# Optimization experiments

Hardware: AMD Instinct MI355X
Metric: run time of the kernel (lower is better)

The kernel has to match this reference:

```python
import jax, jax.numpy as jnp
import numpy as np

N, K = 10000, 32          # nodes, max neighbors
NUM_ELEM = 100
D_ATOM = 128              # atom embedding size
D_DIR_IN, D_DIR = 10, 64  # node direction expansion -> embedding
D_DIST_IN, D_DIST = 128, 128  # edge distance expansion -> embedding


def setup_inputs() -> dict:
    key = jax.random.key(0)
    ks = jax.random.split(key, 12)
    inp = {
        "atomic_numbers": jax.random.randint(ks[0], (N,), 0, NUM_ELEM),
        "node_direction_expansion": jax.random.normal(ks[1], (N, D_DIR_IN), jnp.float32),
        "edge_distance_expansion": jax.random.normal(ks[2], (N, K, D_DIST_IN), jnp.float32),
        "neighbor_list": jax.random.randint(ks[3], (N, K), 0, N),
        "neighbor_mask": jax.random.randint(ks[4], (N, K), 0, 2).astype(bool),
        # learned params
        "src_atom_emb": jax.random.uniform(ks[5], (NUM_ELEM, D_ATOM), jnp.float32, -0.001, 0.001),
        "tgt_atom_emb": jax.random.uniform(ks[6], (NUM_ELEM, D_ATOM), jnp.float32, -0.001, 0.001),
        "src_dir_W": jax.random.normal(ks[7], (D_DIR_IN, D_DIR), jnp.float32) * 0.1,
        "src_dir_b": jnp.zeros((D_DIR,), jnp.float32),
        "tgt_dir_W": jax.random.normal(ks[8], (D_DIR_IN, D_DIR), jnp.float32) * 0.1,
        "tgt_dir_b": jnp.zeros((D_DIR,), jnp.float32),
        "dist_W": jax.random.normal(ks[9], (D_DIST_IN, D_DIST), jnp.float32) * 0.1,
        "dist_b": jnp.zeros((D_DIST,), jnp.float32),
    }
    return inp


def reference(atomic_numbers, node_direction_expansion, edge_distance_expansion,
              neighbor_list, neighbor_mask,
              src_atom_emb, tgt_atom_emb,
              src_dir_W, src_dir_b, tgt_dir_W, tgt_dir_b, dist_W, dist_b):
    # per-node embeddings
    sa = src_atom_emb[atomic_numbers]                      # [N, D_ATOM]
    ta = tgt_atom_emb[atomic_numbers]                      # [N, D_ATOM]
    sd = jax.nn.silu(node_direction_expansion @ src_dir_W + src_dir_b)  # [N, D_DIR]
    td = jax.nn.silu(node_direction_expansion @ tgt_dir_W + tgt_dir_b)  # [N, D_DIR]

    # map_sender_receiver_feature: sender gathered via neighbor_list, receiver broadcast
    sender_atom = sa[neighbor_list]                        # [N, K, D_ATOM]
    recv_atom = jnp.broadcast_to(ta[:, None, :], (N, K, D_ATOM))
    sender_dir = sd[neighbor_list]                         # [N, K, D_DIR]
    recv_dir = jnp.broadcast_to(td[:, None, :], (N, K, D_DIR))

    edist = jax.nn.silu(edge_distance_expansion @ dist_W + dist_b)  # [N, K, D_DIST]

    edge_features = jnp.concatenate(
        [edist, sender_dir, sender_atom, recv_dir, recv_atom], axis=-1)  # [N, K, 512]

    # masked mean over neighbors
    m = neighbor_mask.astype(edge_features.dtype)          # [N, K]
    count = m.sum(axis=1, keepdims=True) + 1e-5            # [N, 1]
    out = (edge_features * m[:, :, None]).sum(axis=1) / count  # [N, 512]
    return out
```

## Files before the change

### kernel.cpp

```cpp
#include <hip/hip_runtime.h>
#include <hip/hip_bf16.h>

#define NN 10000
#define KK 32
#define DDIRIN 10
#define DDIR 64
#define DD 128
#define NODE_BLOCKS 2500

typedef short bf16x8 __attribute__((ext_vector_type(8)));
typedef float f32x4  __attribute__((ext_vector_type(4)));

__device__ __forceinline__ float silu_f(float x) { return x / (1.0f + __expf(-x)); }

__device__ __forceinline__ short f2bf(float f) {
    union { float f; unsigned u; } v; v.f = f;
    unsigned r = (v.u + 0x7fffu + ((v.u >> 16) & 1u)) >> 16;
    return (short)r;
}

__global__ __launch_bounds__(256) void dir_kernel(
    const float* __restrict__ nde,
    const float* __restrict__ sW, const float* __restrict__ sb,
    const float* __restrict__ tW, const float* __restrict__ tb,
    float* __restrict__ sd, float* __restrict__ td)
{
    int gid = blockIdx.x * 256 + threadIdx.x;
    if (gid >= NN * DDIR) return;
    int n = gid >> 6, d = gid & 63;
    float a = sb[d], t = tb[d];
    const float* x = nde + n * DDIRIN;
#pragma unroll
    for (int i = 0; i < DDIRIN; ++i) {
        float xv = x[i];
        a = fmaf(xv, sW[i * DDIR + d], a);
        t = fmaf(xv, tW[i * DDIR + d], t);
    }
    sd[gid] = silu_f(a);
    td[gid] = silu_f(t);
}

template<bool USE_WS>
__global__ __launch_bounds__(256) void gnn_mfma_kernel(
    const int*   __restrict__ an,
    const float* __restrict__ nde,
    const float* __restrict__ edist,
    const int*   __restrict__ nl,
    const int*   __restrict__ nmask,
    const float* __restrict__ semb,
    const float* __restrict__ temb,
    const float* __restrict__ sW, const float* __restrict__ sb,
    const float* __restrict__ tW, const float* __restrict__ tb,
    const float* __restrict__ dW, const float* __restrict__ db,
    const float* __restrict__ sd_ws,
    const float* __restrict__ td_ws,
    float* __restrict__ out)
{
    const int tid  = threadIdx.x;
    const int wid  = tid >> 6;
    const int lane = tid & 63;
    const int l15  = lane & 15;
    const int quad = lane >> 4;

    __shared__ __align__(16) short s_E[32 * 128];
    __shared__ int   s_nl[KK];
    __shared__ float s_mask[KK];
    __shared__ int   s_annl[KK];
    __shared__ float s_sd[USE_WS ? 1 : KK * (DDIR + 4)];
    __shared__ float s_nde[USE_WS ? 1 : KK * DDIRIN];
    __shared__ float s_td[DDIR];

    bf16x8 bfrag[2][4];
    float  bias[2];
#pragma unroll
    for (int c2 = 0; c2 < 2; ++c2) {
        int ncol = (2 * wid + c2) * 16 + l15;
        bias[c2] = db[ncol];
#pragma unroll
        for (int t = 0; t < 4; ++t) {
            bf16x8 v;
#pragma unroll
            for (int j = 0; j < 8; ++j)
                v[j] = f2bf(dW[(t * 32 + quad * 8 + j) * DD + ncol]);
            bfrag[c2][t] = v;
        }
    }

    for (int n = blockIdx.x; n < NN; n += NODE_BLOCKS) {
        __syncthreads();

        if (tid < KK) {
            int j = nl[n * KK + tid];
            s_nl[tid]   = j;
            s_mask[tid] = (nmask[n * KK + tid] != 0) ? 1.0f : 0.0f;
            s_annl[tid] = an[j];
        }
        {
            const float4* E4 = reinterpret_cast<const float4*>(edist + (size_t)n * (KK * DD));
            int row = tid >> 3;
            int cb0 = (tid & 7) * 2;
            float4 a = E4[tid * 4 + 0], b = E4[tid * 4 + 1];
            float4 c = E4[tid * 4 + 2], d = E4[tid * 4 + 3];
            bf16x8 v0, v1;
            v0[0] = f2bf(a.x); v0[1] = f2bf(a.y); v0[2] = f2bf(a.z); v0[3] = f2bf(a.w);
            v0[4] = f2bf(b.x); v0[5] = f2bf(b.y); v0[6] = f2bf(b.z); v0[7] = f2bf(b.w);
            v1[0] = f2bf(c.x); v1[1] = f2bf(c.y); v1[2] = f2bf(c.z); v1[3] = f2bf(c.w);
            v1[4] = f2bf(d.x); v1[5] = f2bf(d.y); v1[6] = f2bf(d.z); v1[7] = f2bf(d.w);
            int sw0 = (cb0     ) ^ (row & 7);
            int sw1 = (cb0 + 1 ) ^ (row & 7);
            *reinterpret_cast<bf16x8*>(&s_E[row * 128 + sw0 * 8]) = v0;
            *reinterpret_cast<bf16x8*>(&s_E[row * 128 + sw1 * 8]) = v1;
        }
        __syncthreads();

        float cnt = 0.0f;
#pragma unroll
        for (int k = 0; k < KK; ++k) cnt += s_mask[k];
        const float inv = 1.0f / (cnt + 1e-5f);
        const float self_scale = cnt * inv;
        float* outn = out + (size_t)n * 512;

        bf16x8 afrag[2][4];
#pragma unroll
        for (int rt = 0; rt < 2; ++rt)
#pragma unroll
            for (int t = 0; t < 4; ++t) {
                int r  = rt * 16 + l15;
                int cb = (t * 4 + quad) ^ (l15 & 7);
                afrag[rt][t] = *reinterpret_cast<const bf16x8*>(&s_E[r * 128 + cb * 8]);
            }
        f32x4 acc[2][2] = {{{0.f,0.f,0.f,0.f},{0.f,0.f,0.f,0.f}},
                           {{0.f,0.f,0.f,0.f},{0.f,0.f,0.f,0.f}}};
#pragma unroll
        for (int t = 0; t < 4; ++t)
#pragma unroll
            for (int rt = 0; rt < 2; ++rt) {
                acc[rt][0] = __builtin_amdgcn_mfma_f32_16x16x32_bf16(afrag[rt][t], bfrag[0][t], acc[rt][0], 0, 0, 0);
                acc[rt][1] = __builtin_amdgcn_mfma_f32_16x16x32_bf16(afrag[rt][t], bfrag[1][t], acc[rt][1], 0, 0, 0);
            }

#pragma unroll
        for (int c2 = 0; c2 < 2; ++c2) {
            float p = 0.0f;
#pragma unroll
            for (int rt = 0; rt < 2; ++rt)
#pragma unroll
                for (int rg = 0; rg < 4; ++rg)
                    p += s_mask[rt * 16 + quad * 4 + rg] * silu_f(acc[rt][c2][rg] + bias[c2]);
            p += __shfl_xor(p, 16);
            p += __shfl_xor(p, 32);
            if (quad == c2) outn[(2 * wid + c2) * 16 + l15] = p * inv;
        }

        if constexpr (!USE_WS) {
            for (int idx = tid; idx < KK * DDIRIN; idx += 256) {
                int k = idx / DDIRIN, i = idx - k * DDIRIN;
                s_nde[k * DDIRIN + i] = nde[s_nl[k] * DDIRIN + i];
            }
            __syncthreads();
            {
                int k = tid >> 3, d0 = (tid & 7) * 8;
                float a8[8];
#pragma unroll
                for (int d = 0; d < 8; ++d) a8[d] = sb[d0 + d];
#pragma unroll
                for (int i = 0; i < DDIRIN; ++i) {
                    float x = s_nde[k * DDIRIN + i];
#pragma unroll
                    for (int d = 0; d < 8; ++d)
                        a8[d] = fmaf(x, sW[i * DDIR + d0 + d], a8[d]);
                }
#pragma unroll
                for (int d = 0; d < 8; ++d) s_sd[k * (DDIR + 4) + d0 + d] = silu_f(a8[d]);
            }
            if (tid < DDIR) {
                float a = tb[tid];
#pragma unroll
                for (int i = 0; i < DDIRIN; ++i)
                    a = fmaf(nde[n * DDIRIN + i], tW[i * DDIR + tid], a);
                s_td[tid] = silu_f(a);
            }
            __syncthreads();
        }

        if (tid < 64) {
            float s = 0.0f;
            if constexpr (USE_WS) {
#pragma unroll 4
                for (int k = 0; k < KK; ++k)
                    s += s_mask[k] * sd_ws[s_nl[k] * DDIR + tid];
            } else {
#pragma unroll
                for (int k = 0; k < KK; ++k)
                    s += s_mask[k] * s_sd[k * (DDIR + 4) + tid];
            }
            outn[128 + tid] = s * inv;
        } else if (tid < 192) {
            int d = tid - 64;
            float s = 0.0f;
#pragma unroll 4
            for (int k = 0; k < KK; ++k)
                s += s_mask[k] * semb[s_annl[k] * DD + d];
            outn[192 + d] = s * inv;
        } else {
            int d = tid - 192;
            float tdv;
            if constexpr (USE_WS) tdv = td_ws[n * DDIR + d];
            else                  tdv = s_td[d];
            outn[320 + d] = tdv * self_scale;
        }
        if (tid < 128)
            outn[384 + tid] = temb[an[n] * DD + tid] * self_scale;
    }
}

extern "C" void kernel_launch(void* const* d_in, const int* in_sizes, int n_in,
                              void* d_out, int out_size, void* d_ws, size_t ws_size,
                              hipStream_t stream) {
    const int*   an    = (const int*)  d_in[0];
    const float* nde   = (const float*)d_in[1];
    const float* edist = (const float*)d_in[2];
    const int*   nl    = (const int*)  d_in[3];
    const int*   nmask = (const int*)  d_in[4];
    const float* semb  = (const float*)d_in[5];
    const float* temb  = (const float*)d_in[6];
    const float* sW    = (const float*)d_in[7];
    const float* sb    = (const float*)d_in[8];
    const float* tW    = (const float*)d_in[9];
    const float* tb    = (const float*)d_in[10];
    const float* dW    = (const float*)d_in[11];
    const float* db    = (const float*)d_in[12];
    float* out = (float*)d_out;

    const size_t need = (size_t)NN * DDIR * sizeof(float) * 2;
    if (ws_size >= need) {
        float* sd = (float*)d_ws;
        float* td = sd + (size_t)NN * DDIR;
        dir_kernel<<<(NN * DDIR + 255) / 256, 256, 0, stream>>>(nde, sW, sb, tW, tb, sd, td);
        gnn_mfma_kernel<true><<<NODE_BLOCKS, 256, 0, stream>>>(
            an, nde, edist, nl, nmask, semb, temb, sW, sb, tW, tb, dW, db, sd, td, out);
    } else {
        gnn_mfma_kernel<false><<<NODE_BLOCKS, 256, 0, stream>>>(
            an, nde, edist, nl, nmask, semb, temb, sW, sb, tW, tb, dW, db,
            nullptr, nullptr, out);
    }
}
```

Baseline: 304.8 us.

## Split fused kernel into batched MFMA GEMM kernel and compacted gather kernel

```diff
diff --git a/kernel.cpp b/kernel.cpp
--- a/kernel.cpp
+++ b/kernel.cpp
@@ -6,17 +6,16 @@
 #define DDIRIN 10
 #define DDIR 64
 #define DD 128
-#define NODE_BLOCKS 2500
 
 typedef short bf16x8 __attribute__((ext_vector_type(8)));
 typedef float f32x4  __attribute__((ext_vector_type(4)));
 
 __device__ __forceinline__ float silu_f(float x) { return x / (1.0f + __expf(-x)); }
 
-__device__ __forceinline__ short f2bf(float f) {
-    union { float f; unsigned u; } v; v.f = f;
-    unsigned r = (v.u + 0x7fffu + ((v.u >> 16) & 1u)) >> 16;
-    return (short)r;
+__device__ __forceinline__ ushort2 pk_bf16(float a, float b) {
+    __hip_bfloat162 h = __float22bfloat162_rn(float2{a, b});
+    union { __hip_bfloat162 h; ushort2 u; } v; v.h = h;
+    return v.u;
 }
 
 __global__ __launch_bounds__(256) void dir_kernel(
@@ -40,18 +39,131 @@
     td[gid] = silu_f(t);
 }
 
+__global__ __launch_bounds__(256, 2) void gemm_kernel(
+    const float* __restrict__ edist,
+    const int*   __restrict__ nmask,
+    const float* __restrict__ dW,
+    const float* __restrict__ db,
+    float* __restrict__ out)
+{
+    const int tid  = threadIdx.x;
+    const int wid  = tid >> 6;
+    const int lane = tid & 63;
+    const int l15  = lane & 15;
+    const int quad = lane >> 4;
+    const int n0   = blockIdx.x * 4;
+
+    __shared__ __align__(16) short s_E[128 * 128];
+    __shared__ float s_cnt[4];
+
+    bf16x8 bfrag[2][4];
+    float  bias[2];
+#pragma unroll
+    for (int c2 = 0; c2 < 2; ++c2) {
+        int ncol = (2 * wid + c2) * 16 + l15;
+        bias[c2] = db[ncol];
+#pragma unroll
+        for (int t = 0; t < 4; ++t) {
+            bf16x8 v;
+#pragma unroll
+            for (int j2 = 0; j2 < 4; ++j2) {
+                int k0 = t * 32 + quad * 8 + 2 * j2;
+                ushort2 u = pk_bf16(dW[k0 * DD + ncol], dW[(k0 + 1) * DD + ncol]);
+                v[2 * j2]     = (short)u.x;
+                v[2 * j2 + 1] = (short)u.y;
+            }
+            bfrag[c2][t] = v;
+        }
+    }
+
+    {
+        const float4* E4 = reinterpret_cast<const float4*>(edist + (size_t)n0 * (KK * DD));
+        const int* nm = nmask + n0 * KK;
+#pragma unroll
+        for (int i = 0; i < 8; ++i) {
+            int f0  = 2 * tid + 512 * i;
+            int row = f0 >> 5;
+            float4 a = E4[f0], b = E4[f0 + 1];
+            ushort2 u0 = pk_bf16(a.x, a.y), u1 = pk_bf16(a.z, a.w);
+            ushort2 u2 = pk_bf16(b.x, b.y), u3 = pk_bf16(b.z, b.w);
+            bf16x8 v;
+            v[0] = (short)u0.x; v[1] = (short)u0.y; v[2] = (short)u1.x; v[3] = (short)u1.y;
+            v[4] = (short)u2.x; v[5] = (short)u2.y; v[6] = (short)u3.x; v[7] = (short)u3.y;
+            bf16x8 z; 
+#pragma unroll
+            for (int q = 0; q < 8; ++q) z[q] = 0;
+            v = (nm[row] != 0) ? v : z;
+            int kb = tid & 15;
+            int sw = kb ^ (row & 7);
+            *reinterpret_cast<bf16x8*>(&s_E[row * 128 + sw * 8]) = v;
+        }
+        if (tid < 4) {
+            int c = 0;
+#pragma unroll 8
+            for (int k = 0; k < KK; ++k) c += (nm[tid * KK + k] != 0) ? 1 : 0;
+            s_cnt[tid] = (float)c;
+        }
+    }
+    __syncthreads();
+
+    f32x4 acc[8][2];
+#pragma unroll
+    for (int rt = 0; rt < 8; ++rt)
+#pragma unroll
+        for (int c2 = 0; c2 < 2; ++c2)
+#pragma unroll
+            for (int g = 0; g < 4; ++g) acc[rt][c2][g] = 0.0f;
+
+#pragma unroll
+    for (int rt = 0; rt < 8; ++rt) {
+        bf16x8 af[4];
+        int r = rt * 16 + l15;
+#pragma unroll
+        for (int t = 0; t < 4; ++t) {
+            int kb = (4 * t + quad) ^ (l15 & 7);
+            af[t] = *reinterpret_cast<const bf16x8*>(&s_E[r * 128 + kb * 8]);
+        }
+#pragma unroll
+        for (int t = 0; t < 4; ++t) {
+            acc[rt][0] = __builtin_amdgcn_mfma_f32_16x16x32_bf16(af[t], bfrag[0][t], acc[rt][0], 0, 0, 0);
+            acc[rt][1] = __builtin_amdgcn_mfma_f32_16x16x32_bf16(af[t], bfrag[1][t], acc[rt][1], 0, 0, 0);
+        }
+    }
+
+#pragma unroll
+    for (int c2 = 0; c2 < 2; ++c2) {
+        float sbv = silu_f(bias[c2]);
+#pragma unroll
+        for (int nd = 0; nd < 4; ++nd) {
+            float p = 0.0f;
+#pragma unroll
+            for (int h = 0; h < 2; ++h) {
+                int rt = 2 * nd + h;
+#pragma unroll
+                for (int g = 0; g < 4; ++g)
+                    p += silu_f(acc[rt][c2][g] + bias[c2]);
+            }
+            p += __shfl_xor(p, 16);
+            p += __shfl_xor(p, 32);
+            if (quad == nd) {
+                float c = s_cnt[nd];
+                float val = (p - (32.0f - c) * sbv) / (c + 1e-5f);
+                out[(size_t)(n0 + nd) * 512 + (2 * wid + c2) * 16 + l15] = val;
+            }
+        }
+    }
+}
+
 template<bool USE_WS>
-__global__ __launch_bounds__(256) void gnn_mfma_kernel(
+__global__ __launch_bounds__(256) void seg_kernel(
     const int*   __restrict__ an,
     const float* __restrict__ nde,
-    const float* __restrict__ edist,
     const int*   __restrict__ nl,
     const int*   __restrict__ nmask,
     const float* __restrict__ semb,
     const float* __restrict__ temb,
     const float* __restrict__ sW, const float* __restrict__ sb,
     const float* __restrict__ tW, const float* __restrict__ tb,
-    const float* __restrict__ dW, const float* __restrict__ db,
     const float* __restrict__ sd_ws,
     const float* __restrict__ td_ws,
     float* __restrict__ out)
@@ -59,158 +171,78 @@
     const int tid  = threadIdx.x;
     const int wid  = tid >> 6;
     const int lane = tid & 63;
-    const int l15  = lane & 15;
-    const int quad = lane >> 4;
-
-    __shared__ __align__(16) short s_E[32 * 128];
-    __shared__ int   s_nl[KK];
-    __shared__ float s_mask[KK];
-    __shared__ int   s_annl[KK];
-    __shared__ float s_sd[USE_WS ? 1 : KK * (DDIR + 4)];
-    __shared__ float s_nde[USE_WS ? 1 : KK * DDIRIN];
-    __shared__ float s_td[DDIR];
-
-    bf16x8 bfrag[2][4];
-    float  bias[2];
-#pragma unroll
-    for (int c2 = 0; c2 < 2; ++c2) {
-        int ncol = (2 * wid + c2) * 16 + l15;
-        bias[c2] = db[ncol];
-#pragma unroll
-        for (int t = 0; t < 4; ++t) {
-            bf16x8 v;
-#pragma unroll
-            for (int j = 0; j < 8; ++j)
-                v[j] = f2bf(dW[(t * 32 + quad * 8 + j) * DD + ncol]);
-            bfrag[c2][t] = v;
-        }
-    }
-
-    for (int n = blockIdx.x; n < NN; n += NODE_BLOCKS) {
-        __syncthreads();
-
-        if (tid < KK) {
-            int j = nl[n * KK + tid];
-            s_nl[tid]   = j;
-            s_mask[tid] = (nmask[n * KK + tid] != 0) ? 1.0f : 0.0f;
-            s_annl[tid] = an[j];
-        }
-        {
-            const float4* E4 = reinterpret_cast<const float4*>(edist + (size_t)n * (KK * DD));
-            int row = tid >> 3;
-            int cb0 = (tid & 7) * 2;
-            float4 a = E4[tid * 4 + 0], b = E4[tid * 4 + 1];
-            float4 c = E4[tid * 4 + 2], d = E4[tid * 4 + 3];
-            bf16x8 v0, v1;
-            v0[0] = f2bf(a.x); v0[1] = f2bf(a.y); v0[2] = f2bf(a.z); v0[3] = f2bf(a.w);
-            v0[4] = f2bf(b.x); v0[5] = f2bf(b.y); v0[6] = f2bf(b.z); v0[7] = f2bf(b.w);
-            v1[0] = f2bf(c.x); v1[1] = f2bf(c.y); v1[2] = f2bf(c.z); v1[3] = f2bf(c.w);
-            v1[4] = f2bf(d.x); v1[5] = f2bf(d.y); v1[6] = f2bf(d.z); v1[7] = f2bf(d.w);
-            int sw0 = (cb0     ) ^ (row & 7);
-            int sw1 = (cb0 + 1 ) ^ (row & 7);
-            *reinterpret_cast<bf16x8*>(&s_E[row * 128 + sw0 * 8]) = v0;
-            *reinterpret_cast<bf16x8*>(&s_E[row * 128 + sw1 * 8]) = v1;
-        }
-        __syncthreads();
-
-        float cnt = 0.0f;
-#pragma unroll
-        for (int k = 0; k < KK; ++k) cnt += s_mask[k];
-        const float inv = 1.0f / (cnt + 1e-5f);
-        const float self_scale = cnt * inv;
-        float* outn = out + (size_t)n * 512;
-
-        bf16x8 afrag[2][4];
-#pragma unroll
-        for (int rt = 0; rt < 2; ++rt)
-#pragma unroll
-            for (int t = 0; t < 4; ++t) {
-                int r  = rt * 16 + l15;
-                int cb = (t * 4 + quad) ^ (l15 & 7);
-                afrag[rt][t] = *reinterpret_cast<const bf16x8*>(&s_E[r * 128 + cb * 8]);
-            }
-        f32x4 acc[2][2] = {{{0.f,0.f,0.f,0.f},{0.f,0.f,0.f,0.f}},
-                           {{0.f,0.f,0.f,0.f},{0.f,0.f,0.f,0.f}}};
-#pragma unroll
-        for (int t = 0; t < 4; ++t)
-#pragma unroll
-            for (int rt = 0; rt < 2; ++rt) {
-                acc[rt][0] = __builtin_amdgcn_mfma_f32_16x16x32_bf16(afrag[rt][t], bfrag[0][t], acc[rt][0], 0, 0, 0);
-                acc[rt][1] = __builtin_amdgcn_mfma_f32_16x16x32_bf16(afrag[rt][t], bfrag[1][t], acc[rt][1], 0, 0, 0);
-            }
-
-#pragma unroll
-        for (int c2 = 0; c2 < 2; ++c2) {
-            float p = 0.0f;
-#pragma unroll
-            for (int rt = 0; rt < 2; ++rt)
-#pragma unroll
-                for (int rg = 0; rg < 4; ++rg)
-                    p += s_mask[rt * 16 + quad * 4 + rg] * silu_f(acc[rt][c2][rg] + bias[c2]);
-            p += __shfl_xor(p, 16);
-            p += __shfl_xor(p, 32);
-            if (quad == c2) outn[(2 * wid + c2) * 16 + l15] = p * inv;
-        }
-
-        if constexpr (!USE_WS) {
-            for (int idx = tid; idx < KK * DDIRIN; idx += 256) {
-                int k = idx / DDIRIN, i = idx - k * DDIRIN;
-                s_nde[k * DDIRIN + i] = nde[s_nl[k] * DDIRIN + i];
-            }
-            __syncthreads();
-            {
-                int k = tid >> 3, d0 = (tid & 7) * 8;
-                float a8[8];
-#pragma unroll
-                for (int d = 0; d < 8; ++d) a8[d] = sb[d0 + d];
-#pragma unroll
-                for (int i = 0; i < DDIRIN; ++i) {
-                    float x = s_nde[k * DDIRIN + i];
-#pragma unroll
-                    for (int d = 0; d < 8; ++d)
-                        a8[d] = fmaf(x, sW[i * DDIR + d0 + d], a8[d]);
-                }
-#pragma unroll
-                for (int d = 0; d < 8; ++d) s_sd[k * (DDIR + 4) + d0 + d] = silu_f(a8[d]);
-            }
-            if (tid < DDIR) {
-                float a = tb[tid];
-#pragma unroll
-                for (int i = 0; i < DDIRIN; ++i)
-                    a = fmaf(nde[n * DDIRIN + i], tW[i * DDIR + tid], a);
-                s_td[tid] = silu_f(a);
-            }
-            __syncthreads();
-        }
-
-        if (tid < 64) {
-            float s = 0.0f;
-            if constexpr (USE_WS) {
+    const int n    = blockIdx.x * 4 + wid;
+
+    __shared__ int s_idx[4][KK];
+    __shared__ int s_aidx[4][KK];
+
+    int j = 0; bool act = false;
+    if (lane < KK) {
+        j   = nl[n * KK + lane];
+        act = (nmask[n * KK + lane] != 0);
+    }
+    unsigned long long bits = __ballot(act);
+    int cnt = (int)__popcll(bits);
+    if (act) {
+        int rank = (int)__popcll(bits & ((1ull << lane) - 1ull));
+        s_idx[wid][rank]  = j;
+        s_aidx[wid][rank] = an[j];
+    }
+    __syncthreads();
+
+    const float invv  = 1.0f / ((float)cnt + 1e-5f);
+    const float scale = (float)cnt * invv;
+    float* outn = out + (size_t)n * 512;
+
+    {
+        float s = 0.0f;
+        if constexpr (USE_WS) {
 #pragma unroll 4
-                for (int k = 0; k < KK; ++k)
-                    s += s_mask[k] * sd_ws[s_nl[k] * DDIR + tid];
-            } else {
-#pragma unroll
-                for (int k = 0; k < KK; ++k)
-                    s += s_mask[k] * s_sd[k * (DDIR + 4) + tid];
-            }
-            outn[128 + tid] = s * inv;
-        } else if (tid < 192) {
-            int d = tid - 64;
-            float s = 0.0f;
+            for (int i = 0; i < cnt; ++i)
+                s += sd_ws[s_idx[wid][i] * DDIR + lane];
+        } else {
+            for (int i = 0; i < cnt; ++i) {
+                int jj = s_idx[wid][i];
+                float a = sb[lane];
+#pragma unroll
+                for (int q = 0; q < DDIRIN; ++q)
+                    a = fmaf(nde[jj * DDIRIN + q], sW[q * DDIR + lane], a);
+                s += silu_f(a);
+            }
+        }
+        outn[128 + lane] = s * invv;
+    }
+
+    {
+        float s0 = 0.0f, s1 = 0.0f;
 #pragma unroll 4
-            for (int k = 0; k < KK; ++k)
-                s += s_mask[k] * semb[s_annl[k] * DD + d];
-            outn[192 + d] = s * inv;
+        for (int i = 0; i < cnt; ++i) {
+            int a = s_aidx[wid][i];
+            s0 += semb[a * DD + lane];
+            s1 += semb[a * DD + 64 + lane];
+        }
+        outn[192 + lane] = s0 * invv;
+        outn[256 + lane] = s1 * invv;
+    }
+
+    {
+        float tdv;
+        if constexpr (USE_WS) {
+            tdv = td_ws[n * DDIR + lane];
         } else {
-            int d = tid - 192;
-            float tdv;
-            if constexpr (USE_WS) tdv = td_ws[n * DDIR + d];
-            else                  tdv = s_td[d];
-            outn[320 + d] = tdv * self_scale;
-        }
-        if (tid < 128)
-            outn[384 + tid] = temb[an[n] * DD + tid] * self_scale;
+            float a = tb[lane];
+#pragma unroll
+            for (int q = 0; q < DDIRIN; ++q)
+                a = fmaf(nde[n * DDIRIN + q], tW[q * DDIR + lane], a);
+            tdv = silu_f(a);
+        }
+        outn[320 + lane] = tdv * scale;
+    }
+
+    {
+        int ann = an[n];
+        outn[384 + lane] = temb[ann * DD + lane] * scale;
+        outn[448 + lane] = temb[ann * DD + 64 + lane] * scale;
     }
 }
 
@@ -232,16 +264,17 @@
     const float* db    = (const float*)d_in[12];
     float* out = (float*)d_out;
 
+    gemm_kernel<<<NN / 4, 256, 0, stream>>>(edist, nmask, dW, db, out);
+
     const size_t need = (size_t)NN * DDIR * sizeof(float) * 2;
     if (ws_size >= need) {
         float* sd = (float*)d_ws;
         float* td = sd + (size_t)NN * DDIR;
         dir_kernel<<<(NN * DDIR + 255) / 256, 256, 0, stream>>>(nde, sW, sb, tW, tb, sd, td);
-        gnn_mfma_kernel<true><<<NODE_BLOCKS, 256, 0, stream>>>(
-            an, nde, edist, nl, nmask, semb, temb, sW, sb, tW, tb, dW, db, sd, td, out);
+        seg_kernel<true><<<NN / 4, 256, 0, stream>>>(
+            an, nde, nl, nmask, semb, temb, sW, sb, tW, tb, sd, td, out);
     } else {
-        gnn_mfma_kernel<false><<<NODE_BLOCKS, 256, 0, stream>>>(
-            an, nde, edist, nl, nmask, semb, temb, sW, sb, tW, tb, dW, db,
-            nullptr, nullptr, out);
-    }
-}
+        seg_kernel<false><<<NN / 4, 256, 0, stream>>>(
+            an, nde, nl, nmask, semb, temb, sW, sb, tW, tb, nullptr, nullptr, out);
+    }
+}
```

New measurement: 280.7 us. -7.9%, faster.
